# Kernel tuning notes

Measured on AMD Instinct MI355X. Metric: run time of the kernel, lower is better.

Reference implementation:

```python
import jax, jax.numpy as jnp
import numpy as np

N_HEAD = 16
ROPE_THETA = 10000.0


def setup_inputs() -> dict:
    key = jax.random.key(0)
    k0, k1, k2 = jax.random.split(key, 3)
    B, T, C = 2, 2048, 1024
    s = 0.02  # GPT-2 style init scale
    return {
        "x": jax.random.normal(k0, (B, T, C), jnp.float32),
        "w_attn": jax.random.normal(k1, (C, 3 * C), jnp.float32) * s,
        "b_attn": jnp.zeros((3 * C,), jnp.float32),
        "w_proj": jax.random.normal(k2, (C, C), jnp.float32) * s,
        "b_proj": jnp.zeros((C,), jnp.float32),
    }


def _rope(x):
    # x: [B, H, T, D]; interleaved-pair rotary (lucidrains rotate_queries_or_keys)
    T, D = x.shape[-2], x.shape[-1]
    inv_freq = 1.0 / (ROPE_THETA ** (jnp.arange(0, D, 2, dtype=jnp.float32) / D))
    freqs = jnp.arange(T, dtype=jnp.float32)[:, None] * inv_freq[None, :]  # [T, D/2]
    emb = jnp.repeat(freqs, 2, axis=-1)  # [T, D], each freq duplicated per pair
    cos, sin = jnp.cos(emb), jnp.sin(emb)
    xr = x.reshape(*x.shape[:-1], D // 2, 2)
    x1, x2 = xr[..., 0], xr[..., 1]
    rot = jnp.stack((-x2, x1), axis=-1).reshape(x.shape)  # rotate_half
    return x * cos + rot * sin


def reference(x, w_attn, b_attn, w_proj, b_proj):
    B, T, C = x.shape
    H = N_HEAD
    D = C // H
    qkv = x @ w_attn + b_attn                      # [B, T, 3C]
    q, k, v = jnp.split(qkv, 3, axis=-1)

    def heads(t):
        return t.reshape(B, T, H, D).transpose(0, 2, 1, 3)  # [B, H, T, D]

    q, k, v = heads(q), heads(k), heads(v)
    q = _rope(q)
    k = _rope(k)

    att = jnp.einsum("bhqd,bhkd->bhqk", q, k) * (1.0 / np.sqrt(D))
    causal = jnp.tril(jnp.ones((T, T), dtype=bool))
    att = jnp.where(causal, att, -jnp.inf)
    att = jax.nn.softmax(att, axis=-1)
    y = jnp.einsum("bhqk,bhkd->bhqd", att, v)
    y = y.transpose(0, 2, 1, 3).reshape(B, T, C)
    return y @ w_proj + b_proj
```

## Files before the change

kernel.cpp:

```cpp
#include <hip/hip_runtime.h>
#include <hip/hip_bf16.h>
#include <stdint.h>

typedef __hip_bfloat16 bf16;
typedef __attribute__((ext_vector_type(8))) short bf16x8;
typedef __attribute__((ext_vector_type(4))) float f32x4;

__device__ inline float bf2f(bf16 v) { return __bfloat162float(v); }
__device__ inline bf16 f2bf(float f) { return __float2bfloat16(f); }

__device__ inline void glds16(const void* g, void* l) {
    __builtin_amdgcn_global_load_lds(
        (const __attribute__((address_space(1))) uint32_t*)g,
        (__attribute__((address_space(3))) uint32_t*)l, 16, 0, 0);
}

__global__ __launch_bounds__(256) void conv_x(const float* __restrict__ in,
                                              bf16* __restrict__ out)
{
    size_t i = ((size_t)blockIdx.x * 256 + threadIdx.x) * 8;
    float4 f0 = *(const float4*)(in + i);
    float4 f1 = *(const float4*)(in + i + 4);
    union { bf16x8 v; bf16 e[8]; } u;
    u.e[0] = f2bf(f0.x); u.e[1] = f2bf(f0.y); u.e[2] = f2bf(f0.z); u.e[3] = f2bf(f0.w);
    u.e[4] = f2bf(f1.x); u.e[5] = f2bf(f1.y); u.e[6] = f2bf(f1.z); u.e[7] = f2bf(f1.w);
    *(bf16x8*)(out + i) = u.v;
}

__global__ __launch_bounds__(256) void conv_wt(const float* __restrict__ W,
                                               bf16* __restrict__ Wt, int N, int K)
{
    __shared__ bf16 t[64][72];
    const int n0 = blockIdx.x * 64, k0 = blockIdx.y * 64;
    const int tid = threadIdx.x;
#pragma unroll
    for (int p = 0; p < 4; ++p) {
        int idx = p * 256 + tid;
        int kr = idx >> 4, c4 = idx & 15;
        float4 f = *(const float4*)(W + (size_t)(k0 + kr) * N + n0 + c4 * 4);
        t[kr][c4 * 4 + 0] = f2bf(f.x); t[kr][c4 * 4 + 1] = f2bf(f.y);
        t[kr][c4 * 4 + 2] = f2bf(f.z); t[kr][c4 * 4 + 3] = f2bf(f.w);
    }
    __syncthreads();
#pragma unroll
    for (int p = 0; p < 2; ++p) {
        int idx = p * 256 + tid;
        int nr = idx >> 3, ch = idx & 7;
        union { bf16x8 v; bf16 e[8]; } u;
#pragma unroll
        for (int j = 0; j < 8; ++j) u.e[j] = t[ch * 8 + j][nr];
        *(bf16x8*)(Wt + (size_t)(n0 + nr) * K + k0 + ch * 8) = u.v;
    }
}

__global__ __launch_bounds__(256) void trig_tab(float2* __restrict__ tab)
{
    int gid = blockIdx.x * 256 + threadIdx.x;
    int p = gid & 31, t = gid >> 5;
    float invf = expf(-(float)(2 * p) * (9.210340371976184f / 64.0f));
    float sn, cs;
    sincosf((float)t * invf, &sn, &cs);
    tab[gid] = make_float2(cs, sn);
}

template <bool OUTF32>
__global__ __launch_bounds__(256) void gemm_bt(
    const bf16* __restrict__ A, const bf16* __restrict__ Bt,
    const float* __restrict__ bias, int M, int N, int K, void* __restrict__ outv)
{
    __shared__ __align__(16) bf16 sa[128 * 32];
    __shared__ __align__(16) bf16 sb[128 * 32];

    const int tid  = threadIdx.x;
    const int wave = tid >> 6, lane = tid & 63;
    const int quad = lane >> 4, l16 = lane & 15;
    const int wm = wave >> 1, wn = wave & 1;
    const int row0 = blockIdx.x * 128, n0 = blockIdx.y * 128;

    f32x4 acc[4][4] = {};

    const int sm = wave * 16 + (lane >> 2);
    const int sk = (lane & 3) * 8;
    const bf16* ga = A  + (size_t)(row0 + sm) * K + sk;
    const bf16* gb = Bt + (size_t)(n0  + sm) * K + sk;
    bf16* la = sa + wave * 512;
    bf16* lb = sb + wave * 512;

    for (int k0 = 0; k0 < K; k0 += 32) {
        __syncthreads();
        glds16(ga + k0, la);
        glds16(ga + k0 + (size_t)64 * K, la + 2048);
        glds16(gb + k0, lb);
        glds16(gb + k0 + (size_t)64 * K, lb + 2048);
        __syncthreads();

        bf16x8 af[4], bfr[4];
#pragma unroll
        for (int mi = 0; mi < 4; ++mi)
            af[mi] = *(const bf16x8*)&sa[(wm * 64 + mi * 16 + l16) * 32 + quad * 8];
#pragma unroll
        for (int ni = 0; ni < 4; ++ni)
            bfr[ni] = *(const bf16x8*)&sb[(wn * 64 + ni * 16 + l16) * 32 + quad * 8];
#pragma unroll
        for (int mi = 0; mi < 4; ++mi)
#pragma unroll
            for (int ni = 0; ni < 4; ++ni)
                acc[mi][ni] = __builtin_amdgcn_mfma_f32_16x16x32_bf16(
                    af[mi], bfr[ni], acc[mi][ni], 0, 0, 0);
    }

#pragma unroll
    for (int ni = 0; ni < 4; ++ni) {
        int col = n0 + wn * 64 + ni * 16 + l16;
        float bvv = bias[col];
#pragma unroll
        for (int mi = 0; mi < 4; ++mi) {
#pragma unroll
            for (int r = 0; r < 4; ++r) {
                int row = row0 + wm * 64 + mi * 16 + quad * 4 + r;
                float v = acc[mi][ni][r] + bvv;
                if (OUTF32) ((float*)outv)[(size_t)row * N + col] = v;
                else        ((bf16*)outv)[(size_t)row * N + col] = f2bf(v);
            }
        }
    }
}

__global__ __launch_bounds__(256) void gemm_qkv(
    const bf16* __restrict__ A, const bf16* __restrict__ Bt,
    const float* __restrict__ bias, const float2* __restrict__ tab,
    bf16* __restrict__ qh, bf16* __restrict__ kh, bf16* __restrict__ vc)
{
    const int M = 4096, N = 3072, K = 1024;
    __shared__ __align__(16) bf16 sa[128 * 32];
    __shared__ __align__(16) bf16 sb[128 * 32];

    const int tid  = threadIdx.x;
    const int wave = tid >> 6, lane = tid & 63;
    const int quad = lane >> 4, l16 = lane & 15;
    const int wm = wave >> 1, wn = wave & 1;
    const int row0 = blockIdx.x * 128, n0 = blockIdx.y * 128;

    f32x4 acc[4][4] = {};

    const int sm = wave * 16 + (lane >> 2);
    const int sk = (lane & 3) * 8;
    const bf16* ga = A  + (size_t)(row0 + sm) * K + sk;
    const bf16* gb = Bt + (size_t)(n0  + sm) * K + sk;
    bf16* la = sa + wave * 512;
    bf16* lb = sb + wave * 512;

    for (int k0 = 0; k0 < K; k0 += 32) {
        __syncthreads();
        glds16(ga + k0, la);
        glds16(ga + k0 + (size_t)64 * K, la + 2048);
        glds16(gb + k0, lb);
        glds16(gb + k0 + (size_t)64 * K, lb + 2048);
        __syncthreads();

        bf16x8 af[4], bfr[4];
#pragma unroll
        for (int mi = 0; mi < 4; ++mi)
            af[mi] = *(const bf16x8*)&sa[(wm * 64 + mi * 16 + l16) * 32 + quad * 8];
#pragma unroll
        for (int ni = 0; ni < 4; ++ni)
            bfr[ni] = *(const bf16x8*)&sb[(wn * 64 + ni * 16 + l16) * 32 + quad * 8];
#pragma unroll
        for (int mi = 0; mi < 4; ++mi)
#pragma unroll
            for (int ni = 0; ni < 4; ++ni)
                acc[mi][ni] = __builtin_amdgcn_mfma_f32_16x16x32_bf16(
                    af[mi], bfr[ni], acc[mi][ni], 0, 0, 0);
    }

    const float QS = 0.125f * 1.44269504088896f;
#pragma unroll
    for (int ni = 0; ni < 4; ++ni) {
        int col = n0 + wn * 64 + ni * 16 + l16;
        float bvv = bias[col];
        int sec = col >> 10;
        int cd  = col & 1023;
        int h   = cd >> 6, d = cd & 63;
        int p   = d >> 1;
        bool odd = (d & 1) != 0;
#pragma unroll
        for (int mi = 0; mi < 4; ++mi) {
#pragma unroll
            for (int r = 0; r < 4; ++r) {
                int row = row0 + wm * 64 + mi * 16 + quad * 4 + r;
                float v = acc[mi][ni][r] + bvv;
                float vp = __shfl_xor(v, 1);
                if (sec == 2) {
                    vc[(size_t)row * 1024 + cd] = f2bf(v);
                } else {
                    int tt = row & 2047, b = row >> 11;
                    float2 cssn = tab[tt * 32 + p];
                    float ro = odd ? (v * cssn.x + vp * cssn.y)
                                   : (v * cssn.x - vp * cssn.y);
                    size_t dst = (((size_t)(b * 16 + h)) * 2048 + tt) * 64 + d;
                    if (sec == 0) qh[dst] = f2bf(ro * QS);
                    else          kh[dst] = f2bf(ro);
                }
            }
        }
    }
}

__global__ __launch_bounds__(256) void transpose_v(
    const bf16* __restrict__ vc, bf16* __restrict__ vt)
{
    __shared__ bf16 t[64][72];
    const int t0 = blockIdx.x * 64;
    const int bh = blockIdx.y, b = bh >> 4, h = bh & 15;
    const int tid = threadIdx.x;
#pragma unroll
    for (int p = 0; p < 2; ++p) {
        int idx = p * 256 + tid;
        int tr = idx >> 3, ch = idx & 7;
        bf16x8 v = *(const bf16x8*)(vc + ((size_t)(b * 2048 + t0 + tr)) * 1024
                                    + h * 64 + ch * 8);
#pragma unroll
        for (int j = 0; j < 8; ++j) t[tr][ch * 8 + j] = ((const bf16*)&v)[j];
    }
    __syncthreads();
#pragma unroll
    for (int p = 0; p < 2; ++p) {
        int idx = p * 256 + tid;
        int dr = idx >> 3, ch = idx & 7;
        union { bf16x8 v; bf16 e[8]; } u;
#pragma unroll
        for (int j = 0; j < 8; ++j) u.e[j] = t[ch * 8 + j][dr];
        *(bf16x8*)(vt + ((size_t)bh * 64 + dr) * 2048 + t0 + ch * 8) = u.v;
    }
}

__global__ __launch_bounds__(256) void attn_k(
    const bf16* __restrict__ qg, const bf16* __restrict__ kg,
    const bf16* __restrict__ vtg, bf16* __restrict__ y)
{
    __shared__ __align__(16) bf16 sK[128 * 64];
    __shared__ __align__(16) bf16 sV[64 * 128];
    __shared__ __align__(16) bf16 pL[4][16][136];

    const int tid  = threadIdx.x;
    const int wave = tid >> 6, lane = tid & 63;
    const int quad = lane >> 4, l16 = lane & 15;
    const int bh   = blockIdx.x;
    const int qt   = 31 - (int)blockIdx.y;
    const bf16* Q  = qg  + (size_t)bh * 2048 * 64;
    const bf16* K  = kg  + (size_t)bh * 2048 * 64;
    const bf16* Vt = vtg + (size_t)bh * 64 * 2048;
    const int b = bh >> 4, h = bh & 15;

    const int q0 = qt * 64 + wave * 16;

    bf16x8 aq[2];
    aq[0] = *(const bf16x8*)(Q + (size_t)(q0 + l16) * 64 + quad * 8);
    aq[1] = *(const bf16x8*)(Q + (size_t)(q0 + l16) * 64 + 32 + quad * 8);

    union { bf16x8 v; short e[8]; } uo;
#pragma unroll
    for (int j = 0; j < 8; ++j) uo.e[j] = (short)0x3F80;
    const bf16x8 vones = uo.v;

    f32x4 o[4] = {};
    f32x4 ls   = {};
    float m_r[4] = {-1e30f, -1e30f, -1e30f, -1e30f};
    const float THR = 8.0f;

    for (int kt = 0; kt <= q0 + 15; kt += 128) {
        __syncthreads();
#pragma unroll
        for (int c = 0; c < 4; ++c) {
            int key = wave * 32 + c * 8 + (lane >> 3);
            int p = lane & 7;
            glds16(K + (size_t)(kt + key) * 64 + ((p ^ key) & 7) * 8,
                   &sK[(wave * 32 + c * 8) * 64]);
        }
#pragma unroll
        for (int c = 0; c < 4; ++c) {
            int d = wave * 16 + c * 4 + (lane >> 4);
            int p = lane & 15;
            glds16(Vt + (size_t)d * 2048 + kt + ((p ^ d) & 15) * 8,
                   &sV[(wave * 16 + c * 4) * 128]);
        }
        __syncthreads();

        const int nlast = min(7, (q0 - kt) >> 4);
        f32x4 sc[8];
        __builtin_amdgcn_s_setprio(1);
#pragma unroll
        for (int nt = 0; nt < 8; ++nt) {
            if (nt > nlast) continue;
            int key = nt * 16 + l16;
            f32x4 s0 = {};
            bf16x8 bk0 = *(const bf16x8*)&sK[key * 64 + ((quad ^ key) & 7) * 8];
            s0 = __builtin_amdgcn_mfma_f32_16x16x32_bf16(aq[0], bk0, s0, 0, 0, 0);
            bf16x8 bk1 = *(const bf16x8*)&sK[key * 64 + (((4 + quad) ^ key) & 7) * 8];
            sc[nt] = __builtin_amdgcn_mfma_f32_16x16x32_bf16(aq[1], bk1, s0, 0, 0, 0);
        }
        __builtin_amdgcn_s_setprio(0);
        {
            const int diag = (q0 - kt) >> 4;
            if (diag <= 7) {
                int key = kt + diag * 16 + l16;
#pragma unroll
                for (int r = 0; r < 4; ++r) {
                    int row = q0 + quad * 4 + r;
                    if (key > row) sc[diag][r] = -1e30f;
                }
            }
        }
        float rowmax[4] = {-1e30f, -1e30f, -1e30f, -1e30f};
#pragma unroll
        for (int nt = 0; nt < 8; ++nt) {
            if (nt > nlast) continue;
#pragma unroll
            for (int r = 0; r < 4; ++r) rowmax[r] = fmaxf(rowmax[r], sc[nt][r]);
        }
        bool okl = (rowmax[0] <= m_r[0] + THR) && (rowmax[1] <= m_r[1] + THR) &&
                   (rowmax[2] <= m_r[2] + THR) && (rowmax[3] <= m_r[3] + THR);
        if (!__all((int)okl)) {
#pragma unroll
            for (int off = 1; off < 16; off <<= 1)
#pragma unroll
                for (int r = 0; r < 4; ++r)
                    rowmax[r] = fmaxf(rowmax[r], __shfl_xor(rowmax[r], off));
            float alpha[4];
#pragma unroll
            for (int r = 0; r < 4; ++r) {
                float mn = fmaxf(m_r[r], rowmax[r]);
                alpha[r] = exp2f(m_r[r] - mn);
                m_r[r] = mn;
            }
#pragma unroll
            for (int nt = 0; nt < 4; ++nt)
#pragma unroll
                for (int r = 0; r < 4; ++r) o[nt][r] *= alpha[r];
#pragma unroll
            for (int r = 0; r < 4; ++r) ls[r] *= alpha[r];
        }
#pragma unroll
        for (int nt = 0; nt < 8; ++nt) {
            if (nt > nlast) continue;
#pragma unroll
            for (int r = 0; r < 4; ++r) sc[nt][r] = exp2f(sc[nt][r] - m_r[r]);
        }

#pragma unroll
        for (int nt = 0; nt < 8; ++nt) {
            if (nt > nlast) continue;
            int blk = (2 * nt + (l16 >> 3)) ^ quad;
#pragma unroll
            for (int r = 0; r < 4; ++r)
                pL[wave][quad * 4 + r][blk * 8 + (l16 & 7)] = f2bf(sc[nt][r]);
        }
        if (nlast < 7 && !(nlast & 1)) {
            int blk = (2 * (nlast + 1) + (l16 >> 3)) ^ quad;
#pragma unroll
            for (int r = 0; r < 4; ++r)
                pL[wave][quad * 4 + r][blk * 8 + (l16 & 7)] = f2bf(0.f);
        }
        __builtin_amdgcn_s_setprio(1);
#pragma unroll
        for (int c = 0; c < 4; ++c) {
            if (c > (nlast >> 1)) continue;
            bf16x8 pa = *(const bf16x8*)&pL[wave][l16][(((4 * c + quad) ^ (l16 >> 2)) * 8)];
            ls = __builtin_amdgcn_mfma_f32_16x16x32_bf16(pa, vones, ls, 0, 0, 0);
#pragma unroll
            for (int dnt = 0; dnt < 4; ++dnt) {
                int d = dnt * 16 + l16;
                int cc = c * 4 + quad;
                bf16x8 vb = *(const bf16x8*)&sV[d * 128 + ((cc ^ d) & 15) * 8];
                o[dnt] = __builtin_amdgcn_mfma_f32_16x16x32_bf16(pa, vb, o[dnt], 0, 0, 0);
            }
        }
        __builtin_amdgcn_s_setprio(0);
    }

#pragma unroll
    for (int r = 0; r < 4; ++r) {
        float inv = 1.0f / ls[r];
        int qq = q0 + quad * 4 + r;
#pragma unroll
        for (int nt = 0; nt < 4; ++nt) {
            int d = nt * 16 + l16;
            y[((size_t)(b * 2048 + qq)) * 1024 + h * 64 + d] = f2bf(o[nt][r] * inv);
        }
    }
}

extern "C" void kernel_launch(void* const* d_in, const int* in_sizes, int n_in,
                              void* d_out, int out_size, void* d_ws, size_t ws_size,
                              hipStream_t stream) {
    const float* x      = (const float*)d_in[0];
    const float* w_attn = (const float*)d_in[1];
    const float* b_attn = (const float*)d_in[2];
    const float* w_proj = (const float*)d_in[3];
    const float* b_proj = (const float*)d_in[4];
    float* out = (float*)d_out;

    bf16* xbf = (bf16*)d_ws;
    bf16* wat = xbf + (size_t)4194304;
    bf16* wpt = wat + (size_t)3145728;
    float2* tab = (float2*)(wpt + (size_t)1048576);
    bf16* qh  = wpt + (size_t)1048576 + 262144;
    bf16* kh  = qh  + (size_t)4194304;
    bf16* vc  = kh  + (size_t)4194304;
    bf16* vt  = vc  + (size_t)4194304;
    bf16* yws = vt  + (size_t)4194304;

    dim3 blk(256);
    conv_x<<<dim3(2048), blk, 0, stream>>>(x, xbf);
    conv_wt<<<dim3(48, 16), blk, 0, stream>>>(w_attn, wat, 3072, 1024);
    conv_wt<<<dim3(16, 16), blk, 0, stream>>>(w_proj, wpt, 1024, 1024);
    trig_tab<<<dim3(256), blk, 0, stream>>>(tab);
    gemm_qkv<<<dim3(32, 24), blk, 0, stream>>>(xbf, wat, b_attn, tab, qh, kh, vc);
    transpose_v<<<dim3(32, 32), blk, 0, stream>>>(vc, vt);
    attn_k<<<dim3(32, 32), blk, 0, stream>>>(qh, kh, vt, yws);
    gemm_bt<true><<<dim3(32, 8), blk, 0, stream>>>(yws, wpt, b_proj,
                                                   4096, 1024, 1024, out);
    (void)in_sizes; (void)n_in; (void)ws_size; (void)out_size;
}
```

Baseline: 228.6 us.

## Merge prep kernels and deepen GEMM K-tile to 64 with XOR-swizzled LDS

```diff
diff --git a/kernel.cpp b/kernel.cpp
--- a/kernel.cpp
+++ b/kernel.cpp
@@ -15,24 +15,11 @@
         (__attribute__((address_space(3))) uint32_t*)l, 16, 0, 0);
 }
 
-__global__ __launch_bounds__(256) void conv_x(const float* __restrict__ in,
-                                              bf16* __restrict__ out)
-{
-    size_t i = ((size_t)blockIdx.x * 256 + threadIdx.x) * 8;
-    float4 f0 = *(const float4*)(in + i);
-    float4 f1 = *(const float4*)(in + i + 4);
-    union { bf16x8 v; bf16 e[8]; } u;
-    u.e[0] = f2bf(f0.x); u.e[1] = f2bf(f0.y); u.e[2] = f2bf(f0.z); u.e[3] = f2bf(f0.w);
-    u.e[4] = f2bf(f1.x); u.e[5] = f2bf(f1.y); u.e[6] = f2bf(f1.z); u.e[7] = f2bf(f1.w);
-    *(bf16x8*)(out + i) = u.v;
-}
-
-__global__ __launch_bounds__(256) void conv_wt(const float* __restrict__ W,
-                                               bf16* __restrict__ Wt, int N, int K)
-{
-    __shared__ bf16 t[64][72];
-    const int n0 = blockIdx.x * 64, k0 = blockIdx.y * 64;
-    const int tid = threadIdx.x;
+__device__ inline void conv_wt_tile(const float* __restrict__ W,
+                                    bf16* __restrict__ Wt, int N, int K,
+                                    int bx, int by, int tid, bf16 (*t)[72])
+{
+    const int n0 = bx * 64, k0 = by * 64;
 #pragma unroll
     for (int p = 0; p < 4; ++p) {
         int idx = p * 256 + tid;
@@ -53,14 +40,37 @@
     }
 }
 
-__global__ __launch_bounds__(256) void trig_tab(float2* __restrict__ tab)
-{
-    int gid = blockIdx.x * 256 + threadIdx.x;
-    int p = gid & 31, t = gid >> 5;
-    float invf = expf(-(float)(2 * p) * (9.210340371976184f / 64.0f));
-    float sn, cs;
-    sincosf((float)t * invf, &sn, &cs);
-    tab[gid] = make_float2(cs, sn);
+__global__ __launch_bounds__(256) void prep(
+    const float* __restrict__ x, bf16* __restrict__ xbf,
+    const float* __restrict__ w_attn, bf16* __restrict__ wat,
+    const float* __restrict__ w_proj, bf16* __restrict__ wpt,
+    float2* __restrict__ tab)
+{
+    __shared__ bf16 t[64][72];
+    const int bid = blockIdx.x;
+    const int tid = threadIdx.x;
+    if (bid < 2048) {
+        size_t i = ((size_t)bid * 256 + tid) * 8;
+        float4 f0 = *(const float4*)(x + i);
+        float4 f1 = *(const float4*)(x + i + 4);
+        union { bf16x8 v; bf16 e[8]; } u;
+        u.e[0] = f2bf(f0.x); u.e[1] = f2bf(f0.y); u.e[2] = f2bf(f0.z); u.e[3] = f2bf(f0.w);
+        u.e[4] = f2bf(f1.x); u.e[5] = f2bf(f1.y); u.e[6] = f2bf(f1.z); u.e[7] = f2bf(f1.w);
+        *(bf16x8*)(xbf + i) = u.v;
+    } else if (bid < 2816) {
+        int idx = bid - 2048;
+        conv_wt_tile(w_attn, wat, 3072, 1024, idx % 48, idx / 48, tid, t);
+    } else if (bid < 3072) {
+        int idx = bid - 2816;
+        conv_wt_tile(w_proj, wpt, 1024, 1024, idx % 16, idx / 16, tid, t);
+    } else {
+        int gid = (bid - 3072) * 256 + tid;
+        int p = gid & 31, tt = gid >> 5;
+        float invf = expf(-(float)(2 * p) * (9.210340371976184f / 64.0f));
+        float sn, cs;
+        sincosf((float)tt * invf, &sn, &cs);
+        tab[gid] = make_float2(cs, sn);
+    }
 }
 
 template <bool OUTF32>
@@ -68,8 +78,8 @@
     const bf16* __restrict__ A, const bf16* __restrict__ Bt,
     const float* __restrict__ bias, int M, int N, int K, void* __restrict__ outv)
 {
-    __shared__ __align__(16) bf16 sa[128 * 32];
-    __shared__ __align__(16) bf16 sb[128 * 32];
+    __shared__ __align__(16) bf16 sa[128 * 64];
+    __shared__ __align__(16) bf16 sb[128 * 64];
 
     const int tid  = threadIdx.x;
     const int wave = tid >> 6, lane = tid & 63;
@@ -79,34 +89,45 @@
 
     f32x4 acc[4][4] = {};
 
-    const int sm = wave * 16 + (lane >> 2);
-    const int sk = (lane & 3) * 8;
-    const bf16* ga = A  + (size_t)(row0 + sm) * K + sk;
-    const bf16* gb = Bt + (size_t)(n0  + sm) * K + sk;
-    bf16* la = sa + wave * 512;
-    bf16* lb = sb + wave * 512;
-
-    for (int k0 = 0; k0 < K; k0 += 32) {
-        __syncthreads();
-        glds16(ga + k0, la);
-        glds16(ga + k0 + (size_t)64 * K, la + 2048);
-        glds16(gb + k0, lb);
-        glds16(gb + k0 + (size_t)64 * K, lb + 2048);
-        __syncthreads();
-
-        bf16x8 af[4], bfr[4];
-#pragma unroll
-        for (int mi = 0; mi < 4; ++mi)
-            af[mi] = *(const bf16x8*)&sa[(wm * 64 + mi * 16 + l16) * 32 + quad * 8];
-#pragma unroll
-        for (int ni = 0; ni < 4; ++ni)
-            bfr[ni] = *(const bf16x8*)&sb[(wn * 64 + ni * 16 + l16) * 32 + quad * 8];
-#pragma unroll
-        for (int mi = 0; mi < 4; ++mi)
-#pragma unroll
-            for (int ni = 0; ni < 4; ++ni)
-                acc[mi][ni] = __builtin_amdgcn_mfma_f32_16x16x32_bf16(
-                    af[mi], bfr[ni], acc[mi][ni], 0, 0, 0);
+    const int srow = lane >> 3;
+    const int schk = lane & 7;
+
+    for (int k0 = 0; k0 < K; k0 += 64) {
+        __syncthreads();
+#pragma unroll
+        for (int half = 0; half < 2; ++half) {
+#pragma unroll
+            for (int g = 0; g < 2; ++g) {
+                int rowb = half * 64 + wave * 16 + g * 8;
+                int row  = rowb + srow;
+                glds16(A + (size_t)(row0 + row) * K + k0 + ((schk ^ row) & 7) * 8,
+                       &sa[rowb * 64]);
+                glds16(Bt + (size_t)(n0 + row) * K + k0 + ((schk ^ row) & 7) * 8,
+                       &sb[rowb * 64]);
+            }
+        }
+        __syncthreads();
+
+#pragma unroll
+        for (int kk = 0; kk < 2; ++kk) {
+            bf16x8 af[4], bfr[4];
+#pragma unroll
+            for (int mi = 0; mi < 4; ++mi) {
+                int row = wm * 64 + mi * 16 + l16;
+                af[mi] = *(const bf16x8*)&sa[row * 64 + (((kk * 4 + quad) ^ row) & 7) * 8];
+            }
+#pragma unroll
+            for (int ni = 0; ni < 4; ++ni) {
+                int row = wn * 64 + ni * 16 + l16;
+                bfr[ni] = *(const bf16x8*)&sb[row * 64 + (((kk * 4 + quad) ^ row) & 7) * 8];
+            }
+#pragma unroll
+            for (int mi = 0; mi < 4; ++mi)
+#pragma unroll
+                for (int ni = 0; ni < 4; ++ni)
+                    acc[mi][ni] = __builtin_amdgcn_mfma_f32_16x16x32_bf16(
+                        af[mi], bfr[ni], acc[mi][ni], 0, 0, 0);
+        }
     }
 
 #pragma unroll
@@ -131,9 +152,9 @@
     const float* __restrict__ bias, const float2* __restrict__ tab,
     bf16* __restrict__ qh, bf16* __restrict__ kh, bf16* __restrict__ vc)
 {
-    const int M = 4096, N = 3072, K = 1024;
-    __shared__ __align__(16) bf16 sa[128 * 32];
-    __shared__ __align__(16) bf16 sb[128 * 32];
+    const int K = 1024;
+    __shared__ __align__(16) bf16 sa[128 * 64];
+    __shared__ __align__(16) bf16 sb[128 * 64];
 
     const int tid  = threadIdx.x;
     const int wave = tid >> 6, lane = tid & 63;
@@ -143,34 +164,45 @@
 
     f32x4 acc[4][4] = {};
 
-    const int sm = wave * 16 + (lane >> 2);
-    const int sk = (lane & 3) * 8;
-    const bf16* ga = A  + (size_t)(row0 + sm) * K + sk;
-    const bf16* gb = Bt + (size_t)(n0  + sm) * K + sk;
-    bf16* la = sa + wave * 512;
-    bf16* lb = sb + wave * 512;
-
-    for (int k0 = 0; k0 < K; k0 += 32) {
-        __syncthreads();
-        glds16(ga + k0, la);
-        glds16(ga + k0 + (size_t)64 * K, la + 2048);
-        glds16(gb + k0, lb);
-        glds16(gb + k0 + (size_t)64 * K, lb + 2048);
-        __syncthreads();
-
-        bf16x8 af[4], bfr[4];
-#pragma unroll
-        for (int mi = 0; mi < 4; ++mi)
-            af[mi] = *(const bf16x8*)&sa[(wm * 64 + mi * 16 + l16) * 32 + quad * 8];
-#pragma unroll
-        for (int ni = 0; ni < 4; ++ni)
-            bfr[ni] = *(const bf16x8*)&sb[(wn * 64 + ni * 16 + l16) * 32 + quad * 8];
-#pragma unroll
-        for (int mi = 0; mi < 4; ++mi)
-#pragma unroll
-            for (int ni = 0; ni < 4; ++ni)
-                acc[mi][ni] = __builtin_amdgcn_mfma_f32_16x16x32_bf16(
-                    af[mi], bfr[ni], acc[mi][ni], 0, 0, 0);
+    const int srow = lane >> 3;
+    const int schk = lane & 7;
+
+    for (int k0 = 0; k0 < K; k0 += 64) {
+        __syncthreads();
+#pragma unroll
+        for (int half = 0; half < 2; ++half) {
+#pragma unroll
+            for (int g = 0; g < 2; ++g) {
+                int rowb = half * 64 + wave * 16 + g * 8;
+                int row  = rowb + srow;
+                glds16(A + (size_t)(row0 + row) * K + k0 + ((schk ^ row) & 7) * 8,
+                       &sa[rowb * 64]);
+                glds16(Bt + (size_t)(n0 + row) * K + k0 + ((schk ^ row) & 7) * 8,
+                       &sb[rowb * 64]);
+            }
+        }
+        __syncthreads();
+
+#pragma unroll
+        for (int kk = 0; kk < 2; ++kk) {
+            bf16x8 af[4], bfr[4];
+#pragma unroll
+            for (int mi = 0; mi < 4; ++mi) {
+                int row = wm * 64 + mi * 16 + l16;
+                af[mi] = *(const bf16x8*)&sa[row * 64 + (((kk * 4 + quad) ^ row) & 7) * 8];
+            }
+#pragma unroll
+            for (int ni = 0; ni < 4; ++ni) {
+                int row = wn * 64 + ni * 16 + l16;
+                bfr[ni] = *(const bf16x8*)&sb[row * 64 + (((kk * 4 + quad) ^ row) & 7) * 8];
+            }
+#pragma unroll
+            for (int mi = 0; mi < 4; ++mi)
+#pragma unroll
+                for (int ni = 0; ni < 4; ++ni)
+                    acc[mi][ni] = __builtin_amdgcn_mfma_f32_16x16x32_bf16(
+                        af[mi], bfr[ni], acc[mi][ni], 0, 0, 0);
+        }
     }
 
     const float QS = 0.125f * 1.44269504088896f;
@@ -411,10 +443,7 @@
     bf16* yws = vt  + (size_t)4194304;
 
     dim3 blk(256);
-    conv_x<<<dim3(2048), blk, 0, stream>>>(x, xbf);
-    conv_wt<<<dim3(48, 16), blk, 0, stream>>>(w_attn, wat, 3072, 1024);
-    conv_wt<<<dim3(16, 16), blk, 0, stream>>>(w_proj, wpt, 1024, 1024);
-    trig_tab<<<dim3(256), blk, 0, stream>>>(tab);
+    prep<<<dim3(3328), blk, 0, stream>>>(x, xbf, w_attn, wat, w_proj, wpt, tab);
     gemm_qkv<<<dim3(32, 24), blk, 0, stream>>>(xbf, wat, b_attn, tab, qh, kh, vc);
     transpose_v<<<dim3(32, 32), blk, 0, stream>>>(vc, vt);
     attn_k<<<dim3(32, 32), blk, 0, stream>>>(qh, kh, vt, yws);
```

Result: no change. 232.6 us (+1.7%).
